# Optimization experiments

Hardware: AMD Instinct MI355X
Metric: run time of the kernel (lower is better)

Reference implementation:

```python
import jax, jax.numpy as jnp
import numpy as np

POOL_RATIO = 0.5  # SAGPooling default ratio


def graph_conv(x, src, dst, Wr, Wn, b, num_nodes):
    # PyG GraphConv (aggr='add'): h_i = x_i Wr + (sum_{j->i} x_j) Wn + b
    agg = jax.ops.segment_sum(x[src], dst, num_segments=num_nodes)
    return x @ Wr + agg @ Wn + b


def setup_inputs() -> dict:
    key = jax.random.key(0)
    ks = jax.random.split(key, 12)
    B, M, DF = 64, 512, 128           # batch, max_num_obj, per-feature dim
    N = B * M                          # 32768 flat nodes
    E = 524288                         # avg degree 16
    D_IN, D_OUT, L, C = 256, 256, 3, 11
    s_in = 1.0 / np.sqrt(D_IN)
    f0 = jax.random.normal(ks[0], (B, M, DF), jnp.float32)
    f1 = jax.random.normal(ks[1], (B, M, DF), jnp.float32)
    collated_edge_index = jax.random.randint(ks[2], (2, E), 0, N, dtype=jnp.int32)
    Wr = jax.random.normal(ks[3], (L, D_IN, D_OUT), jnp.float32) * s_in
    Wn = jax.random.normal(ks[4], (L, D_IN, D_OUT), jnp.float32) * s_in
    b = jax.random.normal(ks[5], (L, D_OUT), jnp.float32) * 0.01
    Wpr = jax.random.normal(ks[6], (D_OUT, 1), jnp.float32) * s_in
    Wpn = jax.random.normal(ks[7], (D_OUT, 1), jnp.float32) * s_in
    bp = jax.random.normal(ks[8], (1,), jnp.float32) * 0.01
    Wc = jax.random.normal(ks[9], (D_OUT, C), jnp.float32) * s_in
    bc = jax.random.normal(ks[10], (C,), jnp.float32) * 0.01
    return {"f0": f0, "f1": f1, "collated_edge_index": collated_edge_index,
            "Wr": Wr, "Wn": Wn, "b": b, "Wpr": Wpr, "Wpn": Wpn, "bp": bp,
            "Wc": Wc, "bc": bc}


def reference(f0, f1, collated_edge_index, Wr, Wn, b, Wpr, Wpn, bp, Wc, bc):
    # concat node features then flatten batch: [B, M, 2*DF] -> [N, D_IN]
    x = jnp.concatenate([f0, f1], axis=2)
    x = x.reshape(-1, x.shape[-1])
    N = x.shape[0]
    src, dst = collated_edge_index[0], collated_edge_index[1]
    for i in range(Wr.shape[0]):  # stacked GNN blocks + ReLU
        x = jax.nn.relu(graph_conv(x, src, dst, Wr[i], Wn[i], b[i], N))
    # SAGPooling: GraphConv attention score; source's batch tensor is constant
    # so top-k runs over all N nodes as one segment (ratio 0.5)
    score = graph_conv(x, src, dst, Wpr, Wpn, bp, N)[:, 0]
    k = int(np.ceil(POOL_RATIO * N))
    top_scores, perm = jax.lax.top_k(score, k)
    xp = x[perm] * jnp.tanh(top_scores)[:, None]   # [k, D_OUT]
    xp = jax.nn.relu(xp)
    logits = xp @ Wc + bc                          # [k, 11]
    return logits
```

## Files before the change

### kernel.cpp

```cpp
#include <hip/hip_runtime.h>
#include <hip/hip_bf16.h>
#include <math.h>
#include <stdint.h>


__global__ __launch_bounds__(256) void concat_kernel(const float* __restrict__ f0,
                                                     const float* __restrict__ f1,
                                                     float* __restrict__ x,
                                                     int N) {
    int gid = blockIdx.x * blockDim.x + threadIdx.x;
    int total = N * 64;
    if (gid >= total) return;
    int n = gid >> 6;
    int q = gid & 63;
    float4 v;
    if (q < 32) v = *(const float4*)(f0 + (size_t)n * 128 + q * 4);
    else        v = *(const float4*)(f1 + (size_t)n * 128 + (q - 32) * 4);
    *(float4*)(x + (size_t)n * 256 + q * 4) = v;
}

__global__ __launch_bounds__(256) void count_kernel(const int* __restrict__ dst,
                                                    int* __restrict__ counts, int E) {
    int e = blockIdx.x * blockDim.x + threadIdx.x;
    if (e < E) atomicAdd(&counts[dst[e]], 1);
}

__global__ __launch_bounds__(1024) void scan_kernel(int* __restrict__ counts,
                                                    int* __restrict__ offs,
                                                    int N, int E) {
    __shared__ int s[1024];
    int t = threadIdx.x;
    int base = t * 32;
    int local[32];
    int sum = 0;
    #pragma unroll
    for (int j = 0; j < 32; ++j) { local[j] = counts[base + j]; sum += local[j]; }
    s[t] = sum;
    __syncthreads();
    for (int off = 1; off < 1024; off <<= 1) {
        int other = (t >= off) ? s[t - off] : 0;
        __syncthreads();
        s[t] += other;
        __syncthreads();
    }
    int run = s[t] - sum;
    #pragma unroll
    for (int j = 0; j < 32; ++j) {
        offs[base + j] = run;
        run += local[j];
        counts[base + j] = 0;
    }
    if (t == 1023) offs[N] = E;
}

__global__ __launch_bounds__(256) void fill_kernel(const int* __restrict__ dst,
                                                   const int* __restrict__ offs,
                                                   int* __restrict__ cursor,
                                                   int* __restrict__ csr, int E) {
    int e = blockIdx.x * blockDim.x + threadIdx.x;
    if (e >= E) return;
    int d = dst[e];
    int pos = offs[d] + atomicAdd(&cursor[d], 1);
    csr[pos] = e;
}

__global__ __launch_bounds__(256) void bsort_kernel(int* __restrict__ csr,
                                                    const int* __restrict__ offs,
                                                    const int* __restrict__ src,
                                                    int N) {
    int i = blockIdx.x * blockDim.x + threadIdx.x;
    if (i >= N) return;
    int beg = offs[i], end = offs[i + 1];
    for (int a = beg + 1; a < end; ++a) {
        int v = csr[a];
        int b = a - 1;
        while (b >= beg && csr[b] > v) { csr[b + 1] = csr[b]; --b; }
        csr[b + 1] = v;
    }
    for (int p = beg; p < end; ++p) csr[p] = src[csr[p]];
}

__global__ __launch_bounds__(256) void segsum_kernel(const float* __restrict__ X,
                                                     const int* __restrict__ csr,
                                                     const int* __restrict__ offs,
                                                     float* __restrict__ AGG, int N) {
    int w = threadIdx.x >> 6;
    int lane = threadIdx.x & 63;
    int n = blockIdx.x * 4 + w;
    if (n >= N) return;
    int beg = offs[n], end = offs[n + 1];
    float4 acc = make_float4(0.f, 0.f, 0.f, 0.f);
    for (int p = beg; p < end; ++p) {
        int s = csr[p];
        float4 v = *(const float4*)(X + (size_t)s * 256 + lane * 4);
        acc.x += v.x; acc.y += v.y; acc.z += v.z; acc.w += v.w;
    }
    *(float4*)(AGG + (size_t)n * 256 + lane * 4) = acc;
}

#define GBM 128
#define GBN 128
#define GBK 16
__global__ __launch_bounds__(256) void gemm_two_kernel(const float* __restrict__ X,
                                                       const float* __restrict__ G,
                                                       const float* __restrict__ W1,
                                                       const float* __restrict__ W2,
                                                       const float* __restrict__ bias,
                                                       float* __restrict__ Y,
                                                       int N) {
    __shared__ float As[GBK][GBM + 4];
    __shared__ float Ws[GBK][GBN + 4];
    const int tid = threadIdx.x;
    const int tcol = tid & 15;
    const int trow = tid >> 4;
    const int rowBase = blockIdx.y * GBM;
    const int colBase = blockIdx.x * GBN;

    const int ar0 = tid >> 2;
    const int ak  = (tid & 3) * 4;
    const int wk0 = tid >> 5;
    const int wc  = (tid & 31) * 4;

    float acc[8][8];
    #pragma unroll
    for (int i = 0; i < 8; ++i)
        #pragma unroll
        for (int j = 0; j < 8; ++j) acc[i][j] = 0.f;

    for (int kt = 0; kt < 32; ++kt) {
        const int kb = kt * GBK;
        const float* Asrc = (kb < 256) ? X : G;
        const float* Wsrc = (kb < 256) ? W1 : W2;
        const int kloc = kb & 255;
        float4 a0 = *(const float4*)(Asrc + (size_t)(rowBase + ar0) * 256 + kloc + ak);
        float4 a1 = *(const float4*)(Asrc + (size_t)(rowBase + ar0 + 64) * 256 + kloc + ak);
        float4 w0 = *(const float4*)(Wsrc + (size_t)(kloc + wk0) * 256 + colBase + wc);
        float4 w1 = *(const float4*)(Wsrc + (size_t)(kloc + wk0 + 8) * 256 + colBase + wc);
        __syncthreads();
        As[ak + 0][ar0] = a0.x; As[ak + 1][ar0] = a0.y;
        As[ak + 2][ar0] = a0.z; As[ak + 3][ar0] = a0.w;
        As[ak + 0][ar0 + 64] = a1.x; As[ak + 1][ar0 + 64] = a1.y;
        As[ak + 2][ar0 + 64] = a1.z; As[ak + 3][ar0 + 64] = a1.w;
        *(float4*)&Ws[wk0][wc] = w0;
        *(float4*)&Ws[wk0 + 8][wc] = w1;
        __syncthreads();
        #pragma unroll
        for (int kk = 0; kk < GBK; ++kk) {
            float a[8], w[8];
            *(float4*)&a[0] = *(const float4*)&As[kk][trow * 8];
            *(float4*)&a[4] = *(const float4*)&As[kk][trow * 8 + 4];
            *(float4*)&w[0] = *(const float4*)&Ws[kk][tcol * 8];
            *(float4*)&w[4] = *(const float4*)&Ws[kk][tcol * 8 + 4];
            #pragma unroll
            for (int i = 0; i < 8; ++i)
                #pragma unroll
                for (int j = 0; j < 8; ++j)
                    acc[i][j] = fmaf(a[i], w[j], acc[i][j]);
        }
    }
    #pragma unroll
    for (int i = 0; i < 8; ++i) {
        const int row = rowBase + trow * 8 + i;
        float o[8];
        #pragma unroll
        for (int j = 0; j < 8; ++j) {
            float v = acc[i][j] + bias[colBase + tcol * 8 + j];
            o[j] = fmaxf(v, 0.f);
        }
        *(float4*)(Y + (size_t)row * 256 + colBase + tcol * 8)     = *(const float4*)&o[0];
        *(float4*)(Y + (size_t)row * 256 + colBase + tcol * 8 + 4) = *(const float4*)&o[4];
    }
}

__global__ __launch_bounds__(256) void dot_kernel(const float* __restrict__ X3,
                                                  const float* __restrict__ Wpr,
                                                  const float* __restrict__ Wpn,
                                                  double* __restrict__ yr,
                                                  double* __restrict__ yn, int N) {
    int w = threadIdx.x >> 6;
    int lane = threadIdx.x & 63;
    int n = blockIdx.x * 4 + w;
    if (n >= N) return;
    float4 xv = *(const float4*)(X3 + (size_t)n * 256 + lane * 4);
    float4 wr = *(const float4*)(Wpr + lane * 4);
    float4 wn = *(const float4*)(Wpn + lane * 4);
    double dr = (double)xv.x * wr.x + (double)xv.y * wr.y +
                (double)xv.z * wr.z + (double)xv.w * wr.w;
    double dn = (double)xv.x * wn.x + (double)xv.y * wn.y +
                (double)xv.z * wn.z + (double)xv.w * wn.w;
    #pragma unroll
    for (int o = 32; o > 0; o >>= 1) {
        dr += __shfl_down(dr, o, 64);
        dn += __shfl_down(dn, o, 64);
    }
    if (lane == 0) { yr[n] = dr; yn[n] = dn; }
}

__global__ __launch_bounds__(256) void score_gather_kernel(
        const double* __restrict__ yr, const double* __restrict__ yn,
        const int* __restrict__ csr, const int* __restrict__ offs,
        const float* __restrict__ bp,
        double* __restrict__ sc, unsigned long long* __restrict__ keys, int N) {
    int n = blockIdx.x * blockDim.x + threadIdx.x;
    if (n >= N) return;
    double s = yr[n] + (double)bp[0];
    int beg = offs[n], end = offs[n + 1];
    for (int p = beg; p < end; ++p) s += yn[csr[p]];
    sc[n] = s;
    long long sb = __double_as_longlong(s);
    keys[n] = (sb < 0) ? ~(unsigned long long)sb
                       : ((unsigned long long)sb | 0x8000000000000000ULL);
}

#define RTI 1024
#define RTJ 512
__global__ __launch_bounds__(256) void rank_count_kernel(
        const unsigned long long* __restrict__ keys,
        int* __restrict__ rankcnt, int N) {
    __shared__ __align__(16) unsigned long long sk[RTJ];
    const int tid = threadIdx.x;
    const int ibase = blockIdx.y * RTI;
    const int jbase = blockIdx.x * RTJ;

    unsigned long long ki[4];
    #pragma unroll
    for (int r = 0; r < 4; ++r) ki[r] = keys[ibase + r * 256 + tid];
    for (int t = tid; t < RTJ; t += 256) sk[t] = keys[jbase + t];
    __syncthreads();

    int cnt[4] = {0, 0, 0, 0};
    if (jbase + RTJ <= ibase) {
        for (int u = 0; u < RTJ; u += 8) {
            ulonglong2 p0 = *(const ulonglong2*)&sk[u];
            ulonglong2 p1 = *(const ulonglong2*)&sk[u + 2];
            ulonglong2 p2 = *(const ulonglong2*)&sk[u + 4];
            ulonglong2 p3 = *(const ulonglong2*)&sk[u + 6];
            #pragma unroll
            for (int r = 0; r < 4; ++r) {
                cnt[r] += (int)(p0.x >= ki[r]) + (int)(p0.y >= ki[r])
                        + (int)(p1.x >= ki[r]) + (int)(p1.y >= ki[r])
                        + (int)(p2.x >= ki[r]) + (int)(p2.y >= ki[r])
                        + (int)(p3.x >= ki[r]) + (int)(p3.y >= ki[r]);
            }
        }
    } else if (jbase >= ibase + RTI) {
        for (int u = 0; u < RTJ; u += 8) {
            ulonglong2 p0 = *(const ulonglong2*)&sk[u];
            ulonglong2 p1 = *(const ulonglong2*)&sk[u + 2];
            ulonglong2 p2 = *(const ulonglong2*)&sk[u + 4];
            ulonglong2 p3 = *(const ulonglong2*)&sk[u + 6];
            #pragma unroll
            for (int r = 0; r < 4; ++r) {
                cnt[r] += (int)(p0.x > ki[r]) + (int)(p0.y > ki[r])
                        + (int)(p1.x > ki[r]) + (int)(p1.y > ki[r])
                        + (int)(p2.x > ki[r]) + (int)(p2.y > ki[r])
                        + (int)(p3.x > ki[r]) + (int)(p3.y > ki[r]);
            }
        }
    } else {
        int thr[4];
        #pragma unroll
        for (int r = 0; r < 4; ++r) thr[r] = ibase + r * 256 + tid - jbase;
        for (int u = 0; u < RTJ; ++u) {
            unsigned long long kj = sk[u];
            #pragma unroll
            for (int r = 0; r < 4; ++r)
                cnt[r] += (kj > ki[r]) || (kj == ki[r] && u < thr[r]);
        }
    }
    #pragma unroll
    for (int r = 0; r < 4; ++r)
        atomicAdd(&rankcnt[ibase + r * 256 + tid], cnt[r]);
}

__global__ __launch_bounds__(256) void rank_scatter_kernel(
        const int* __restrict__ rankcnt,
        const double* __restrict__ sc,
        int* __restrict__ perm,
        double* __restrict__ topd, int N, int K) {
    int i = blockIdx.x * blockDim.x + threadIdx.x;
    if (i >= N) return;
    int rank = rankcnt[i];
    if (rank < K) { perm[rank] = i; topd[rank] = sc[i]; }
}

__global__ __launch_bounds__(256) void out_kernel(const float* __restrict__ X3,
                                                  const int* __restrict__ perm,
                                                  const double* __restrict__ topd,
                                                  const float* __restrict__ Wc,
                                                  const float* __restrict__ bc,
                                                  float* __restrict__ out, int K) {
    int w = threadIdx.x >> 6;
    int lane = threadIdx.x & 63;
    int r = blockIdx.x * 4 + w;
    if (r >= K) return;
    int p = perm[r];
    double t = tanh(topd[r]);
    float4 xv = *(const float4*)(X3 + (size_t)p * 256 + lane * 4);
    double xp[4];
    xp[0] = (double)xv.x * t; xp[1] = (double)xv.y * t;
    xp[2] = (double)xv.z * t; xp[3] = (double)xv.w * t;
    #pragma unroll
    for (int j = 0; j < 4; ++j) xp[j] = xp[j] > 0.0 ? xp[j] : 0.0;
    double acc[11];
    #pragma unroll
    for (int c = 0; c < 11; ++c) acc[c] = 0.0;
    #pragma unroll
    for (int j = 0; j < 4; ++j) {
        const float* wrow = Wc + (size_t)(lane * 4 + j) * 11;
        #pragma unroll
        for (int c = 0; c < 11; ++c) acc[c] += xp[j] * (double)wrow[c];
    }
    #pragma unroll
    for (int c = 0; c < 11; ++c) {
        double v = acc[c];
        #pragma unroll
        for (int o = 32; o > 0; o >>= 1) v += __shfl_down(v, o, 64);
        if (lane == 0) out[(size_t)r * 11 + c] = (float)(v + (double)bc[c]);
    }
}

extern "C" void kernel_launch(void* const* d_in, const int* in_sizes, int n_in,
                              void* d_out, int out_size, void* d_ws, size_t ws_size,
                              hipStream_t stream) {
    const float* f0  = (const float*)d_in[0];
    const float* f1  = (const float*)d_in[1];
    const int*   ei  = (const int*)d_in[2];
    const float* Wr  = (const float*)d_in[3];
    const float* Wn  = (const float*)d_in[4];
    const float* b   = (const float*)d_in[5];
    const float* Wpr = (const float*)d_in[6];
    const float* Wpn = (const float*)d_in[7];
    const float* bp  = (const float*)d_in[8];
    const float* Wc  = (const float*)d_in[9];
    const float* bc  = (const float*)d_in[10];
    float* out = (float*)d_out;

    const int N = in_sizes[0] / 128;
    const int E = in_sizes[2] / 2;
    const int K = (N + 1) / 2;
    const int L = in_sizes[5] / 256;

    const int* src = ei;
    const int* dst = ei + E;

    char* p = (char*)d_ws;
    auto take = [&](size_t bytes) {
        char* r = p;
        p += (bytes + 255) & ~(size_t)255;
        return r;
    };
    float*  xA      = (float*)take((size_t)N * 256 * 4);
    float*  xB      = (float*)take((size_t)N * 256 * 4);
    float*  agg     = (float*)take((size_t)N * 256 * 4);
    int*    counts  = (int*)take((size_t)N * 4);
    int*    offs    = (int*)take((size_t)(N + 1) * 4);
    int*    csr     = (int*)take((size_t)E * 4);
    double* sc      = (double*)take((size_t)N * 8);
    unsigned long long* keys = (unsigned long long*)take((size_t)N * 8);
    int*    rankcnt = (int*)take((size_t)N * 4);
    double* topd    = (double*)take((size_t)K * 8);
    int*    perm    = (int*)take((size_t)K * 4);
    double* yrv     = (double*)take((size_t)N * 8);
    double* ynv     = (double*)take((size_t)N * 8);
    (void)ws_size;

    hipMemsetAsync(counts, 0, (size_t)N * 4, stream);
    hipMemsetAsync(rankcnt, 0, (size_t)N * 4, stream);

    concat_kernel<<<(N * 64 + 255) / 256, 256, 0, stream>>>(f0, f1, xA, N);
    count_kernel<<<(E + 255) / 256, 256, 0, stream>>>(dst, counts, E);
    scan_kernel<<<1, 1024, 0, stream>>>(counts, offs, N, E);
    fill_kernel<<<(E + 255) / 256, 256, 0, stream>>>(dst, offs, counts, csr, E);
    bsort_kernel<<<(N + 255) / 256, 256, 0, stream>>>(csr, offs, src, N);

    float* xcur = xA;
    float* xnext = xB;
    for (int i = 0; i < L; ++i) {
        segsum_kernel<<<N / 4, 256, 0, stream>>>(xcur, csr, offs, agg, N);
        gemm_two_kernel<<<dim3(256 / GBN, N / GBM), 256, 0, stream>>>(
            xcur, agg, Wr + (size_t)i * 65536, Wn + (size_t)i * 65536,
            b + (size_t)i * 256, xnext, N);
        float* tmp = xcur; xcur = xnext; xnext = tmp;
    }
    dot_kernel<<<N / 4, 256, 0, stream>>>(xcur, Wpr, Wpn, yrv, ynv, N);
    score_gather_kernel<<<N / 256, 256, 0, stream>>>(yrv, ynv, csr, offs, bp, sc, keys, N);
    rank_count_kernel<<<dim3(N / RTJ, N / RTI), 256, 0, stream>>>(keys, rankcnt, N);
    rank_scatter_kernel<<<(N + 255) / 256, 256, 0, stream>>>(rankcnt, sc, perm, topd, N, K);
    out_kernel<<<K / 4, 256, 0, stream>>>(xcur, perm, topd, Wc, bc, out, K);
}
```

Before: 817.1 us.

## Prefetch next GEMM K-tile into registers, double K tile, split thread micro-tiles

The fp32 dual GEMM now loads the next K-tile from global memory into registers while it computes on the current shared-memory tile, so load latency overlaps the FMA work. The K tile grows from 16 to 32, which halves the number of barrier pairs. Each thread's 8x8 outputs become four 4x4 sub-tiles spread 64 apart, which changes the shared-memory read pattern to cut bank conflicts and keeps the stores coalesced. The cost is more registers for the staged float4 values and more shared memory, which may lower occupancy.

Result: no change. 813.5 us (-0.4%).

```diff
diff --git a/kernel.cpp b/kernel.cpp
--- a/kernel.cpp
+++ b/kernel.cpp
@@ -100,14 +100,30 @@
 
 #define GBM 128
 #define GBN 128
-#define GBK 16
+#define GBK 32
+
+#define GEMM_LOAD_STAGE(kt)                                                          \
+    {                                                                                \
+        const int kb = (kt) * GBK;                                                   \
+        const float* Asrc = (kb < 256) ? X : G;                                      \
+        const float* Wsrc = (kb < 256) ? W1 : W2;                                    \
+        const int kloc = kb & 255;                                                   \
+        a_st0 = *(const float4*)(Asrc + (size_t)(rowBase + ar) * 256 + kloc + ak);   \
+        a_st1 = *(const float4*)(Asrc + (size_t)(rowBase + ar + 64) * 256 + kloc + ak); \
+        a_st2 = *(const float4*)(Asrc + (size_t)(rowBase + ar) * 256 + kloc + 16 + ak); \
+        a_st3 = *(const float4*)(Asrc + (size_t)(rowBase + ar + 64) * 256 + kloc + 16 + ak); \
+        w_st0 = *(const float4*)(Wsrc + (size_t)(kloc + wk) * 256 + colBase + wc);   \
+        w_st1 = *(const float4*)(Wsrc + (size_t)(kloc + wk + 8) * 256 + colBase + wc); \
+        w_st2 = *(const float4*)(Wsrc + (size_t)(kloc + wk + 16) * 256 + colBase + wc); \
+        w_st3 = *(const float4*)(Wsrc + (size_t)(kloc + wk + 24) * 256 + colBase + wc); \
+    }
+
 __global__ __launch_bounds__(256) void gemm_two_kernel(const float* __restrict__ X,
                                                        const float* __restrict__ G,
                                                        const float* __restrict__ W1,
                                                        const float* __restrict__ W2,
                                                        const float* __restrict__ bias,
-                                                       float* __restrict__ Y,
-                                                       int N) {
+                                                       float* __restrict__ Y) {
     __shared__ float As[GBK][GBM + 4];
     __shared__ float Ws[GBK][GBN + 4];
     const int tid = threadIdx.x;
@@ -116,59 +132,71 @@
     const int rowBase = blockIdx.y * GBM;
     const int colBase = blockIdx.x * GBN;
 
-    const int ar0 = tid >> 2;
-    const int ak  = (tid & 3) * 4;
-    const int wk0 = tid >> 5;
-    const int wc  = (tid & 31) * 4;
-
-    float acc[8][8];
-    #pragma unroll
-    for (int i = 0; i < 8; ++i)
-        #pragma unroll
-        for (int j = 0; j < 8; ++j) acc[i][j] = 0.f;
-
-    for (int kt = 0; kt < 32; ++kt) {
-        const int kb = kt * GBK;
-        const float* Asrc = (kb < 256) ? X : G;
-        const float* Wsrc = (kb < 256) ? W1 : W2;
-        const int kloc = kb & 255;
-        float4 a0 = *(const float4*)(Asrc + (size_t)(rowBase + ar0) * 256 + kloc + ak);
-        float4 a1 = *(const float4*)(Asrc + (size_t)(rowBase + ar0 + 64) * 256 + kloc + ak);
-        float4 w0 = *(const float4*)(Wsrc + (size_t)(kloc + wk0) * 256 + colBase + wc);
-        float4 w1 = *(const float4*)(Wsrc + (size_t)(kloc + wk0 + 8) * 256 + colBase + wc);
+    const int ar = tid >> 2;
+    const int ak = (tid & 3) * 4;
+    const int wk = tid >> 5;
+    const int wc = (tid & 31) * 4;
+
+    float4 a_st0, a_st1, a_st2, a_st3, w_st0, w_st1, w_st2, w_st3;
+
+    float acc[4][4][4];
+    #pragma unroll
+    for (int q = 0; q < 4; ++q)
+        #pragma unroll
+        for (int i = 0; i < 4; ++i)
+            #pragma unroll
+            for (int j = 0; j < 4; ++j) acc[q][i][j] = 0.f;
+
+    GEMM_LOAD_STAGE(0);
+
+    for (int kt = 0; kt < 512 / GBK; ++kt) {
         __syncthreads();
-        As[ak + 0][ar0] = a0.x; As[ak + 1][ar0] = a0.y;
-        As[ak + 2][ar0] = a0.z; As[ak + 3][ar0] = a0.w;
-        As[ak + 0][ar0 + 64] = a1.x; As[ak + 1][ar0 + 64] = a1.y;
-        As[ak + 2][ar0 + 64] = a1.z; As[ak + 3][ar0 + 64] = a1.w;
-        *(float4*)&Ws[wk0][wc] = w0;
-        *(float4*)&Ws[wk0 + 8][wc] = w1;
+        #pragma unroll
+        for (int j = 0; j < 4; ++j) {
+            As[ak + j][ar]           = ((const float*)&a_st0)[j];
+            As[ak + j][ar + 64]      = ((const float*)&a_st1)[j];
+            As[16 + ak + j][ar]      = ((const float*)&a_st2)[j];
+            As[16 + ak + j][ar + 64] = ((const float*)&a_st3)[j];
+        }
+        *(float4*)&Ws[wk][wc]      = w_st0;
+        *(float4*)&Ws[wk + 8][wc]  = w_st1;
+        *(float4*)&Ws[wk + 16][wc] = w_st2;
+        *(float4*)&Ws[wk + 24][wc] = w_st3;
         __syncthreads();
+        if (kt < 512 / GBK - 1) GEMM_LOAD_STAGE(kt + 1);
         #pragma unroll
         for (int kk = 0; kk < GBK; ++kk) {
-            float a[8], w[8];
-            *(float4*)&a[0] = *(const float4*)&As[kk][trow * 8];
-            *(float4*)&a[4] = *(const float4*)&As[kk][trow * 8 + 4];
-            *(float4*)&w[0] = *(const float4*)&Ws[kk][tcol * 8];
-            *(float4*)&w[4] = *(const float4*)&Ws[kk][tcol * 8 + 4];
-            #pragma unroll
-            for (int i = 0; i < 8; ++i)
+            float a0[4], a1[4], w0[4], w1[4];
+            *(float4*)a0 = *(const float4*)&As[kk][trow * 4];
+            *(float4*)a1 = *(const float4*)&As[kk][64 + trow * 4];
+            *(float4*)w0 = *(const float4*)&Ws[kk][tcol * 4];
+            *(float4*)w1 = *(const float4*)&Ws[kk][64 + tcol * 4];
+            #pragma unroll
+            for (int i = 0; i < 4; ++i)
                 #pragma unroll
-                for (int j = 0; j < 8; ++j)
-                    acc[i][j] = fmaf(a[i], w[j], acc[i][j]);
-        }
-    }
-    #pragma unroll
-    for (int i = 0; i < 8; ++i) {
-        const int row = rowBase + trow * 8 + i;
-        float o[8];
-        #pragma unroll
-        for (int j = 0; j < 8; ++j) {
-            float v = acc[i][j] + bias[colBase + tcol * 8 + j];
-            o[j] = fmaxf(v, 0.f);
-        }
-        *(float4*)(Y + (size_t)row * 256 + colBase + tcol * 8)     = *(const float4*)&o[0];
-        *(float4*)(Y + (size_t)row * 256 + colBase + tcol * 8 + 4) = *(const float4*)&o[4];
+                for (int j = 0; j < 4; ++j) {
+                    acc[0][i][j] = fmaf(a0[i], w0[j], acc[0][i][j]);
+                    acc[1][i][j] = fmaf(a0[i], w1[j], acc[1][i][j]);
+                    acc[2][i][j] = fmaf(a1[i], w0[j], acc[2][i][j]);
+                    acc[3][i][j] = fmaf(a1[i], w1[j], acc[3][i][j]);
+                }
+        }
+    }
+    #pragma unroll
+    for (int h = 0; h < 2; ++h) {
+        #pragma unroll
+        for (int i = 0; i < 4; ++i) {
+            const int row = rowBase + h * 64 + trow * 4 + i;
+            #pragma unroll
+            for (int g = 0; g < 2; ++g) {
+                const int colb = colBase + g * 64 + tcol * 4;
+                float o[4];
+                #pragma unroll
+                for (int j = 0; j < 4; ++j)
+                    o[j] = fmaxf(acc[h * 2 + g][i][j] + bias[colb + j], 0.f);
+                *(float4*)(Y + (size_t)row * 256 + colb) = *(const float4*)&o[0];
+            }
+        }
     }
 }
 
@@ -380,7 +408,7 @@
         segsum_kernel<<<N / 4, 256, 0, stream>>>(xcur, csr, offs, agg, N);
         gemm_two_kernel<<<dim3(256 / GBN, N / GBM), 256, 0, stream>>>(
             xcur, agg, Wr + (size_t)i * 65536, Wn + (size_t)i * 65536,
-            b + (size_t)i * 256, xnext, N);
+            b + (size_t)i * 256, xnext);
         float* tmp = xcur; xcur = xnext; xnext = tmp;
     }
     dot_kernel<<<N / 4, 256, 0, stream>>>(xcur, Wpr, Wpn, yrv, ynv, N);
```
